# Kernel optimization log

Measured on AMD Instinct MI355X. Metric: run time of the kernel, lower is better.

The kernel has to match this reference:

```python
import jax, jax.numpy as jnp
import numpy as np

B, S, D, H = 8, 128, 256, 8
T = S + 1
HD = D // H  # head_dim = 32
GAMMA = 1.0
NEG_INF = -1e9
LN_EPS = 1e-5


def setup_inputs() -> dict:
    key = jax.random.key(0)
    ks = jax.random.split(key, 16)
    sc = 0.05
    return {
        "desc_embeddings": jax.random.normal(ks[0], (B, S, D), jnp.float32),
        "name_value_embeddings": jax.random.normal(ks[1], (B, T, D), jnp.float32),
        "prior_Q": jax.random.uniform(ks[2], (B, H, S, S), jnp.float32),
        "Wq": jax.random.normal(ks[3], (D, D), jnp.float32) * sc,
        "bq": jnp.zeros((D,), jnp.float32),
        "Wk": jax.random.normal(ks[4], (D, D), jnp.float32) * sc,
        "bk": jnp.zeros((D,), jnp.float32),
        "Wv": jax.random.normal(ks[5], (D, D), jnp.float32) * sc,
        "bv": jnp.zeros((D,), jnp.float32),
        "wa": jax.random.normal(ks[6], (3 * HD,), jnp.float32) * sc,  # attn_proj weight (out=1)
        "ba": jnp.zeros((), jnp.float32),
        "We1": jax.random.normal(ks[7], (2 * D, D), jnp.float32) * sc,
        "be1": jnp.zeros((D,), jnp.float32),
        "ln_g": jnp.ones((D,), jnp.float32),
        "ln_b": jnp.zeros((D,), jnp.float32),
        "We2": jax.random.normal(ks[8], (D, D), jnp.float32) * sc,
        "be2": jnp.zeros((D,), jnp.float32),
    }


def _layer_norm(x, g, b):
    mu = jnp.mean(x, axis=-1, keepdims=True)
    var = jnp.mean(jnp.square(x - mu), axis=-1, keepdims=True)
    return (x - mu) * jax.lax.rsqrt(var + LN_EPS) * g + b


def _heads(x, W, b):  # [B,T,D] -> [B,H,T,HD]
    return (x @ W + b).reshape(B, T, H, HD).transpose(0, 2, 1, 3)


def reference(desc_embeddings, name_value_embeddings, prior_Q,
              Wq, bq, Wk, bk, Wv, bv, wa, ba,
              We1, be1, ln_g, ln_b, We2, be2):
    # structural adjacency (same for every batch element): CLS->Var on, Var->CLS off,
    # Var-Var fully connected without self-loops
    adj = jnp.zeros((T, T), jnp.float32)
    adj = adj.at[1:, 1:].set(1.0 - jnp.eye(S, dtype=jnp.float32))
    adj = adj.at[0, 1:].set(1.0)

    q = _heads(name_value_embeddings, Wq, bq)  # [B,H,T,HD]
    k = _heads(name_value_embeddings, Wk, bk)
    v = _heads(name_value_embeddings, Wv, bv)

    # edge attributes: pairwise concat of desc embeddings, CLS rows/cols use [desc,desc]
    desc = desc_embeddings
    var_edge = jnp.concatenate([
        jnp.broadcast_to(desc[:, :, None, :], (B, S, S, D)),
        jnp.broadcast_to(desc[:, None, :, :], (B, S, S, D)),
    ], axis=-1)  # [B,S,S,2D]
    cls_edge = jnp.concatenate([desc, desc], axis=-1)  # [B,S,2D]
    edge = jnp.zeros((B, T, T, 2 * D), jnp.float32)
    edge = edge.at[:, 1:, 1:].set(var_edge)
    edge = edge.at[:, 0, 1:].set(cls_edge)
    edge = edge.at[:, 1:, 0].set(cls_edge)

    # edge_update MLP: Linear(2D->D) -> LayerNorm -> ReLU -> Linear(D->D)
    h = jax.nn.relu(_layer_norm(edge @ We1 + be1, ln_g, ln_b)) @ We2 + be2  # [B,T,T,D]
    # split into heads, mask by adjacency: [B,H,T,T,HD]
    edge_h = h.reshape(B, T, T, H, HD).transpose(0, 3, 1, 2, 4)
    edge_h = edge_h * adj[None, None, :, :, None]

    # gat_v1 + attn_proj(cat[q_i, k_j, e_ij]) is linear -> decompose to avoid
    # materializing the [B,H,T,T,3*HD] concat
    wa_q, wa_k, wa_e = wa[:HD], wa[HD:2 * HD], wa[2 * HD:]
    logits = (jnp.einsum('bhid,d->bhi', q, wa_q)[:, :, :, None]
              + jnp.einsum('bhjd,d->bhj', k, wa_k)[:, :, None, :]
              + jnp.einsum('bhijd,d->bhij', edge_h, wa_e)
              + ba)  # [B,H,T,T]

    # prior_Q logit-bias injection on Var-Var block
    eps = 1e-6
    p = jnp.clip(prior_Q, eps, 1.0 - eps)
    bias = (jnp.log(p) - jnp.log(1.0 - p)) * GAMMA  # [B,H,S,S]
    logits = logits.at[:, :, 1:, 1:].add(bias)

    # structural mask as pre-softmax -inf
    logits = logits + (adj == 0).astype(logits.dtype)[None, None] * NEG_INF

    attn = jax.nn.softmax(logits, axis=-1)  # [B,H,T,T]
    ctx = jnp.einsum('bhij,bhjd->bhid', attn, v)  # [B,H,T,HD]
    basis_outputs = ctx.transpose(0, 2, 1, 3)  # [B,T,H,HD]
    return basis_outputs, attn
```

## Files before the change

kernel.cpp:

```cpp
#include <hip/hip_runtime.h>
#include <math.h>

#define B 8
#define S 128
#define D 256
#define H 8
#define T 129
#define HD 32
#define BT (B*T)
#define NEG_INF -1000000000.0f
#define LN_EPS 1e-5f

__global__ __launch_bounds__(256) void prep_w(
    const float* __restrict__ Wq, const float* __restrict__ bq,
    const float* __restrict__ Wk, const float* __restrict__ bk,
    const float* __restrict__ We2, const float* __restrict__ be2,
    const float* __restrict__ wa,
    float* __restrict__ Wqk, float* __restrict__ bqk,
    float* __restrict__ W2aT, float* __restrict__ econst)
{
    int id = blockIdx.x * 256 + threadIdx.x;
    if (id < 2048) {
        int c = id >> 3, h = id & 7;
        float s = 0.f;
        #pragma unroll
        for (int d = 0; d < HD; ++d) s = fmaf(Wq[c*D + h*HD + d], wa[d], s);
        Wqk[c*16 + h] = s;
    } else if (id < 4096) {
        int id2 = id - 2048; int c = id2 >> 3, h = id2 & 7;
        float s = 0.f;
        #pragma unroll
        for (int d = 0; d < HD; ++d) s = fmaf(Wk[c*D + h*HD + d], wa[HD + d], s);
        Wqk[c*16 + 8 + h] = s;
    } else if (id < 6144) {
        int id2 = id - 4096; int h = id2 / D, c = id2 % D;
        float s = 0.f;
        #pragma unroll
        for (int d = 0; d < HD; ++d) s = fmaf(We2[c*D + h*HD + d], wa[2*HD + d], s);
        W2aT[h*D + c] = s;
    } else if (id < 6152) {
        int h = id - 6144;
        float s = 0.f;
        #pragma unroll
        for (int d = 0; d < HD; ++d) s = fmaf(bq[h*HD + d], wa[d], s);
        bqk[h] = s;
    } else if (id < 6160) {
        int h = id - 6152;
        float s = 0.f;
        #pragma unroll
        for (int d = 0; d < HD; ++d) s = fmaf(bk[h*HD + d], wa[HD + d], s);
        bqk[8 + h] = s;
    } else if (id < 6168) {
        int h = id - 6160;
        float s = 0.f;
        #pragma unroll
        for (int d = 0; d < HD; ++d) s = fmaf(be2[h*HD + d], wa[2*HD + d], s);
        econst[h] = s;
    }
}

__global__ __launch_bounds__(256) void gemm3(
    const float* __restrict__ nv, const float* __restrict__ desc,
    const float* __restrict__ Wv, const float* __restrict__ bv,
    const float* __restrict__ We1, const float* __restrict__ be1,
    const float* __restrict__ Wqk, const float* __restrict__ bqk,
    float* __restrict__ v, float* __restrict__ U, float* __restrict__ V,
    float* __restrict__ sU, float* __restrict__ sV, float* __restrict__ qdkdT)
{
    const int which = blockIdx.y;
    const int tid = threadIdx.x;
    __shared__ float xs[16][D];
    __shared__ float psum[4][8];

    if (which == 3) {
        if (blockIdx.x >= 65) return;
        const int r0 = blockIdx.x * 16;
        const int r = tid >> 4, c = tid & 15;
        for (int t = tid; t < 16 * D; t += 256) {
            int rr = r0 + (t >> 8);
            xs[t >> 8][t & 255] = (rr < BT) ? nv[rr * D + (t & 255)] : 0.f;
        }
        __syncthreads();
        float acc = 0.f;
        for (int kk = 0; kk < D; kk += 4) {
            float4 x = *(const float4*)&xs[r][kk];
            acc = fmaf(x.x, Wqk[(kk+0)*16 + c], acc);
            acc = fmaf(x.y, Wqk[(kk+1)*16 + c], acc);
            acc = fmaf(x.z, Wqk[(kk+2)*16 + c], acc);
            acc = fmaf(x.w, Wqk[(kk+3)*16 + c], acc);
        }
        const int rr = r0 + r;
        if (rr < BT) qdkdT[c*BT + rr] = acc + bqk[c];
        return;
    }

    const float* X; const float* W; const float* bias; float* out; int rows;
    if (which == 0)      { X = nv;   W = Wv;        bias = bv;  out = v; rows = BT; }
    else if (which == 1) { X = desc; W = We1;       bias = be1; out = U; rows = B*S; }
    else                 { X = desc; W = We1 + D*D; bias = nullptr; out = V; rows = B*S; }

    const int r0 = blockIdx.x * 8;
    if (r0 >= rows) return;

    #pragma unroll
    for (int r = 0; r < 8; ++r) {
        int rr = r0 + r;
        xs[r][tid] = (rr < rows) ? X[rr * D + tid] : 0.f;
    }
    __syncthreads();

    float acc[8] = {0.f,0.f,0.f,0.f,0.f,0.f,0.f,0.f};
    for (int kk = 0; kk < D; kk += 4) {
        float w0 = W[(kk+0)*D + tid];
        float w1 = W[(kk+1)*D + tid];
        float w2 = W[(kk+2)*D + tid];
        float w3 = W[(kk+3)*D + tid];
        #pragma unroll
        for (int r = 0; r < 8; ++r) {
            float4 x = *(const float4*)&xs[r][kk];
            acc[r] = fmaf(x.x, w0, acc[r]);
            acc[r] = fmaf(x.y, w1, acc[r]);
            acc[r] = fmaf(x.z, w2, acc[r]);
            acc[r] = fmaf(x.w, w3, acc[r]);
        }
    }
    const float bb = bias ? bias[tid] : 0.f;
    #pragma unroll
    for (int r = 0; r < 8; ++r) {
        int rr = r0 + r;
        if (rr < rows) out[rr * D + tid] = acc[r] + bb;
    }

    if (which >= 1) {
        const int wv = tid >> 6, ln = tid & 63;
        #pragma unroll
        for (int r = 0; r < 8; ++r) {
            float sps = acc[r] + bb;
            #pragma unroll
            for (int m = 32; m >= 1; m >>= 1) sps += __shfl_xor(sps, m);
            if (ln == 0) psum[wv][r] = sps;
        }
        __syncthreads();
        if (tid < 8) {
            float* dst = (which == 1) ? sU : sV;
            dst[r0 + tid] = psum[0][tid] + psum[1][tid] + psum[2][tid] + psum[3][tid];
        }
    }
}

__global__ __launch_bounds__(512, 4) void edge_attn(
    const float* __restrict__ U, const float* __restrict__ V,
    const float* __restrict__ W2aT, const float* __restrict__ econst,
    const float* __restrict__ ln_g, const float* __restrict__ ln_b,
    const float* __restrict__ qdkdT, const float* __restrict__ prior,
    const float* __restrict__ v, const float* __restrict__ ba,
    const float* __restrict__ sU, const float* __restrict__ sV,
    float* __restrict__ out_basis, float* __restrict__ out_attn)
{
    const int bid = blockIdx.x;
    const int b = bid / T, i = bid % T;
    const int tid = threadIdx.x, lane = tid & 63, wid = tid >> 6;
    const int c0 = lane * 4;

    __shared__ float escl[H][132];
    __shared__ float pat[H][132];

    const int h = wid;
    const int bh = b*H + h;
    const int j1 = 1 + lane, j2 = 65 + lane;
    const float qdv = qdkdT[h*BT + b*T + i];
    const float ba0 = ba[0];
    const float* kT = qdkdT + (8 + h)*BT + b*T;
    const float k1 = kT[j1], k2 = kT[j2];
    float lg1 = 0.f, lg2 = 0.f;
    if (i >= 1) {
        float pr = prior[((size_t)bh*S + (i-1))*S + (j1-1)];
        pr = fminf(fmaxf(pr, 1e-6f), 1.f - 1e-6f);
        lg1 = __logf(pr) - __logf(1.f - pr);
        pr = prior[((size_t)bh*S + (i-1))*S + (j2-1)];
        pr = fminf(fmaxf(pr, 1e-6f), 1.f - 1e-6f);
        lg2 = __logf(pr) - __logf(1.f - pr);
    }

    const float4 g4 = *(const float4*)(ln_g + c0);
    const float4 b4 = *(const float4*)(ln_b + c0);
    float4 w[H];
    #pragma unroll
    for (int hh = 0; hh < H; ++hh) w[hh] = *(const float4*)(W2aT + hh*D + c0);

    const bool i0 = (i == 0);
    float4 u4i = make_float4(0.f, 0.f, 0.f, 0.f);
    float sUi_s = 0.f;
    if (!i0) {
        u4i = *(const float4*)(U + (size_t)(b*S + (i-1))*D + c0);
        sUi_s = sU[b*S + (i-1)];
    }

    const bool bb0 = lane & 1, bb1 = lane & 2, bb2 = lane & 4;
    const bool bb3 = lane & 8, bb4 = lane & 16;
    const int hmap = 4*(lane&1) + 2*((lane>>1)&1) + ((lane>>2)&1);
    const float ech = econst[hmap];

    const int j0 = 1 + wid * 16;
    const float* Vb  = V + (size_t)(b*S + (j0-1))*D + c0;
    const float* Ub  = U + (size_t)(b*S + (j0-1))*D + c0;
    const float* sVb = sV + b*S + (j0-1);
    const float* sUb = sU + b*S + (j0-1);

    #pragma unroll 2
    for (int grp = 0; grp < 4; ++grp) {
        const int jb = grp * 4;
        float4 y0 = *(const float4*)(Vb + (size_t)(jb+0)*D);
        float4 y1 = *(const float4*)(Vb + (size_t)(jb+1)*D);
        float4 y2 = *(const float4*)(Vb + (size_t)(jb+2)*D);
        float4 y3 = *(const float4*)(Vb + (size_t)(jb+3)*D);
        const float4 sv4 = *(const float4*)(sVb + jb);
        float su0 = sUi_s, su1 = sUi_s, su2 = sUi_s, su3 = sUi_s;
        float4 u0 = u4i, u1 = u4i, u2 = u4i, u3 = u4i;
        if (i0) {
            u0 = *(const float4*)(Ub + (size_t)(jb+0)*D);
            u1 = *(const float4*)(Ub + (size_t)(jb+1)*D);
            u2 = *(const float4*)(Ub + (size_t)(jb+2)*D);
            u3 = *(const float4*)(Ub + (size_t)(jb+3)*D);
            const float4 su4 = *(const float4*)(sUb + jb);
            su0 = su4.x; su1 = su4.y; su2 = su4.z; su3 = su4.w;
        }
        y0.x += u0.x; y0.y += u0.y; y0.z += u0.z; y0.w += u0.w;
        y1.x += u1.x; y1.y += u1.y; y1.z += u1.z; y1.w += u1.w;
        y2.x += u2.x; y2.y += u2.y; y2.z += u2.z; y2.w += u2.w;
        y3.x += u3.x; y3.y += u3.y; y3.z += u3.z; y3.w += u3.w;

        float s2p0 = fmaf(y0.x,y0.x, fmaf(y0.y,y0.y, fmaf(y0.z,y0.z, y0.w*y0.w)));
        float s2p1 = fmaf(y1.x,y1.x, fmaf(y1.y,y1.y, fmaf(y1.z,y1.z, y1.w*y1.w)));
        float s2p2 = fmaf(y2.x,y2.x, fmaf(y2.y,y2.y, fmaf(y2.z,y2.z, y2.w*y2.w)));
        float s2p3 = fmaf(y3.x,y3.x, fmaf(y3.y,y3.y, fmaf(y3.z,y3.z, y3.w*y3.w)));
        float a0 = bb0 ? s2p2 : s2p0, d0 = bb0 ? s2p0 : s2p2;
        float a1 = bb0 ? s2p3 : s2p1, d1 = bb0 ? s2p1 : s2p3;
        float r0 = a0 + __shfl_xor(d0, 1);
        float r1 = a1 + __shfl_xor(d1, 1);
        float a2 = bb1 ? r1 : r0, d2 = bb1 ? r0 : r1;
        float z = a2 + __shfl_xor(d2, 2);
        z += __shfl_xor(z, 4);
        z += __shfl_xor(z, 8);
        z += __shfl_xor(z, 16);
        z += __shfl_xor(z, 32);
        const float mu0 = (su0 + sv4.x) * (1.f/D);
        const float mu1 = (su1 + sv4.y) * (1.f/D);
        const float mu2 = (su2 + sv4.z) * (1.f/D);
        const float mu3 = (su3 + sv4.w) * (1.f/D);
        const float musel = bb0 ? (bb1 ? mu3 : mu2) : (bb1 ? mu1 : mu0);
        const float var = fmaf(-musel, musel, z * (1.f/D));
        const float rsv = rsqrtf(var + LN_EPS);
        const float rA = __shfl_xor(rsv, 1);
        const float rB = __shfl_xor(rsv, 2);
        const float rC = __shfl_xor(rA, 2);
        const float rs0 = bb0 ? (bb1 ? rC : rA) : (bb1 ? rB : rsv);
        const float rs1 = bb0 ? (bb1 ? rA : rC) : (bb1 ? rsv : rB);
        const float rs2 = bb0 ? (bb1 ? rB : rsv) : (bb1 ? rC : rA);
        const float rs3 = bb0 ? (bb1 ? rsv : rB) : (bb1 ? rA : rC);

        float x0, x1, x2, x3;
        #define DO_J(YK, RSK, MUK, XOUT)                                          \
        {                                                                         \
            const float rg0 = RSK * g4.x, rg1 = RSK * g4.y;                       \
            const float rg2 = RSK * g4.z, rg3 = RSK * g4.w;                       \
            const float of0 = fmaf(-MUK, rg0, b4.x), of1 = fmaf(-MUK, rg1, b4.y); \
            const float of2 = fmaf(-MUK, rg2, b4.z), of3 = fmaf(-MUK, rg3, b4.w); \
            const float t0 = fmaxf(fmaf(YK.x, rg0, of0), 0.f);                    \
            const float t1 = fmaxf(fmaf(YK.y, rg1, of1), 0.f);                    \
            const float t2 = fmaxf(fmaf(YK.z, rg2, of2), 0.f);                    \
            const float t3 = fmaxf(fmaf(YK.w, rg3, of3), 0.f);                    \
            float ph0 = fmaf(t0, w[0].x, fmaf(t1, w[0].y, fmaf(t2, w[0].z, t3 * w[0].w))); \
            float ph1 = fmaf(t0, w[1].x, fmaf(t1, w[1].y, fmaf(t2, w[1].z, t3 * w[1].w))); \
            float ph2 = fmaf(t0, w[2].x, fmaf(t1, w[2].y, fmaf(t2, w[2].z, t3 * w[2].w))); \
            float ph3 = fmaf(t0, w[3].x, fmaf(t1, w[3].y, fmaf(t2, w[3].z, t3 * w[3].w))); \
            float ph4 = fmaf(t0, w[4].x, fmaf(t1, w[4].y, fmaf(t2, w[4].z, t3 * w[4].w))); \
            float ph5 = fmaf(t0, w[5].x, fmaf(t1, w[5].y, fmaf(t2, w[5].z, t3 * w[5].w))); \
            float ph6 = fmaf(t0, w[6].x, fmaf(t1, w[6].y, fmaf(t2, w[6].z, t3 * w[6].w))); \
            float ph7 = fmaf(t0, w[7].x, fmaf(t1, w[7].y, fmaf(t2, w[7].z, t3 * w[7].w))); \
            float e0 = bb0 ? ph4 : ph0, f0 = bb0 ? ph0 : ph4;                     \
            float e1 = bb0 ? ph5 : ph1, f1 = bb0 ? ph1 : ph5;                     \
            float e2 = bb0 ? ph6 : ph2, f2 = bb0 ? ph2 : ph6;                     \
            float e3 = bb0 ? ph7 : ph3, f3 = bb0 ? ph3 : ph7;                     \
            float p0 = e0 + __shfl_xor(f0, 1);                                    \
            float p1 = e1 + __shfl_xor(f1, 1);                                    \
            float p2 = e2 + __shfl_xor(f2, 1);                                    \
            float p3 = e3 + __shfl_xor(f3, 1);                                    \
            float q0 = (bb1 ? p2 : p0) + __shfl_xor(bb1 ? p0 : p2, 2);            \
            float q1 = (bb1 ? p3 : p1) + __shfl_xor(bb1 ? p1 : p3, 2);            \
            XOUT = (bb2 ? q1 : q0) + __shfl_xor(bb2 ? q0 : q1, 4);                \
        }
        DO_J(y0, rs0, mu0, x0)
        DO_J(y1, rs1, mu1, x1)
        DO_J(y2, rs2, mu2, x2)
        DO_J(y3, rs3, mu3, x3)
        #undef DO_J

        float tA0 = bb3 ? x2 : x0, sA0 = bb3 ? x0 : x2;
        float tA1 = bb3 ? x3 : x1, sA1 = bb3 ? x1 : x3;
        float w0t = tA0 + __shfl_xor(sA0, 8);
        float w1t = tA1 + __shfl_xor(sA1, 8);
        float zz = (bb4 ? w1t : w0t) + __shfl_xor(bb4 ? w0t : w1t, 16);
        zz += __shfl_xor(zz, 32);
        if (lane < 32) {
            const int jm = 2*((lane>>3)&1) + ((lane>>4)&1);
            escl[hmap][j0 + jb + jm] = zz + ech;
        }
    }
    __syncthreads();

    const bool val1 = !(i >= 1 && j1 == i);
    const bool val2 = !(i >= 1 && j2 == i);

    const float base = qdv + ba0;
    const float e1 = val1 ? __expf(base + k1 + escl[h][j1] + lg1) : 0.f;
    const float e2 = val2 ? __expf(base + k2 + escl[h][j2] + lg2) : 0.f;
    float ssum = e1 + e2;
    #pragma unroll
    for (int mm = 32; mm >= 1; mm >>= 1) ssum += __shfl_xor(ssum, mm);
    const float inv = 1.f / ssum;
    const float a1 = e1 * inv, a2 = e2 * inv;

    float* arow = out_attn + (size_t)(bh*T + i)*T;
    arow[j1] = a1;
    arow[j2] = a2;
    if (lane == 0) arow[0] = 0.f;
    pat[h][j1] = a1;
    pat[h][j2] = a2;

    const int dg = lane & 7;
    const int jg = lane >> 3;
    const float* vbase = v + (size_t)(b*T)*D + h*HD + dg*4;
    float4 acc4 = make_float4(0.f, 0.f, 0.f, 0.f);
    #pragma unroll
    for (int k = 0; k < 16; ++k) {
        const int j = 1 + k*8 + jg;
        const float p = pat[h][j];
        const float4 vv = *(const float4*)(vbase + (size_t)j*D);
        acc4.x = fmaf(p, vv.x, acc4.x);
        acc4.y = fmaf(p, vv.y, acc4.y);
        acc4.z = fmaf(p, vv.z, acc4.z);
        acc4.w = fmaf(p, vv.w, acc4.w);
    }
    #pragma unroll
    for (int mm = 8; mm <= 32; mm <<= 1) {
        acc4.x += __shfl_xor(acc4.x, mm);
        acc4.y += __shfl_xor(acc4.y, mm);
        acc4.z += __shfl_xor(acc4.z, mm);
        acc4.w += __shfl_xor(acc4.w, mm);
    }
    if (jg == 0)
        *(float4*)(out_basis + ((size_t)(b*T + i)*H + h)*HD + dg*4) = acc4;
}

extern "C" void kernel_launch(void* const* d_in, const int* in_sizes, int n_in,
                              void* d_out, int out_size, void* d_ws, size_t ws_size,
                              hipStream_t stream) {
    const float* desc  = (const float*)d_in[0];
    const float* nv    = (const float*)d_in[1];
    const float* prior = (const float*)d_in[2];
    const float* Wq  = (const float*)d_in[3];
    const float* bq  = (const float*)d_in[4];
    const float* Wk  = (const float*)d_in[5];
    const float* bk  = (const float*)d_in[6];
    const float* Wv  = (const float*)d_in[7];
    const float* bv  = (const float*)d_in[8];
    const float* wa  = (const float*)d_in[9];
    const float* ba  = (const float*)d_in[10];
    const float* We1 = (const float*)d_in[11];
    const float* be1 = (const float*)d_in[12];
    const float* lng = (const float*)d_in[13];
    const float* lnb = (const float*)d_in[14];
    const float* We2 = (const float*)d_in[15];
    const float* be2 = (const float*)d_in[16];

    float* ws = (float*)d_ws;
    float* U     = ws; ws += B*S*D;
    float* V     = ws; ws += B*S*D;
    float* v     = ws; ws += B*T*D;
    float* Wqk   = ws; ws += D*16;
    float* bqk   = ws; ws += 16;
    float* W2aT  = ws; ws += H*D;
    float* ec    = ws; ws += H;
    float* qdkdT = ws; ws += 16*BT;
    float* sU    = ws; ws += B*S;
    float* sV    = ws; ws += B*S;

    float* out_basis = (float*)d_out;
    float* out_attn  = out_basis + B*T*H*HD;

    prep_w<<<dim3(25), 256, 0, stream>>>(Wq, bq, Wk, bk, We2, be2, wa,
                                         Wqk, bqk, W2aT, ec);
    gemm3<<<dim3(129, 4), 256, 0, stream>>>(nv, desc, Wv, bv, We1, be1,
                                            Wqk, bqk, v, U, V, sU, sV, qdkdT);
    edge_attn<<<dim3(B*T), 512, 0, stream>>>(U, V, W2aT, ec, lng, lnb,
                                             qdkdT, prior, v, ba, sU, sV,
                                             out_basis, out_attn);
}
```

Baseline: 146.5 us.

## Fold weight prep into gemm3 and replace shuffle reduction with shared partial sums

Removes the separate prep_w launch. The per-block q/k attention-weight folding is recomputed redundantly in each gemm3 qdk block into shared memory, and the We2·wa folding runs as an extra blockIdx.y slice. In edge_attn, the final cross-lane shuffle tree for edge scores is replaced by writing per-octet partial sums to a larger shared buffer and summing 8 partials per j. This trades a kernel launch and some shuffles for redundant Wq/Wk reads per block and extra shared memory (about 34 KB) that may lower edge_attn occupancy.

After: 164.4 us. 1.12x slower.

```diff
diff --git a/kernel.cpp b/kernel.cpp
--- a/kernel.cpp
+++ b/kernel.cpp
@@ -11,66 +11,46 @@
 #define NEG_INF -1000000000.0f
 #define LN_EPS 1e-5f
 
-__global__ __launch_bounds__(256) void prep_w(
+__global__ __launch_bounds__(256) void gemm3(
+    const float* __restrict__ nv, const float* __restrict__ desc,
+    const float* __restrict__ Wv, const float* __restrict__ bv,
+    const float* __restrict__ We1, const float* __restrict__ be1,
     const float* __restrict__ Wq, const float* __restrict__ bq,
     const float* __restrict__ Wk, const float* __restrict__ bk,
     const float* __restrict__ We2, const float* __restrict__ be2,
     const float* __restrict__ wa,
-    float* __restrict__ Wqk, float* __restrict__ bqk,
-    float* __restrict__ W2aT, float* __restrict__ econst)
-{
-    int id = blockIdx.x * 256 + threadIdx.x;
-    if (id < 2048) {
-        int c = id >> 3, h = id & 7;
-        float s = 0.f;
-        #pragma unroll
-        for (int d = 0; d < HD; ++d) s = fmaf(Wq[c*D + h*HD + d], wa[d], s);
-        Wqk[c*16 + h] = s;
-    } else if (id < 4096) {
-        int id2 = id - 2048; int c = id2 >> 3, h = id2 & 7;
-        float s = 0.f;
-        #pragma unroll
-        for (int d = 0; d < HD; ++d) s = fmaf(Wk[c*D + h*HD + d], wa[HD + d], s);
-        Wqk[c*16 + 8 + h] = s;
-    } else if (id < 6144) {
-        int id2 = id - 4096; int h = id2 / D, c = id2 % D;
-        float s = 0.f;
-        #pragma unroll
-        for (int d = 0; d < HD; ++d) s = fmaf(We2[c*D + h*HD + d], wa[2*HD + d], s);
-        W2aT[h*D + c] = s;
-    } else if (id < 6152) {
-        int h = id - 6144;
-        float s = 0.f;
-        #pragma unroll
-        for (int d = 0; d < HD; ++d) s = fmaf(bq[h*HD + d], wa[d], s);
-        bqk[h] = s;
-    } else if (id < 6160) {
-        int h = id - 6152;
-        float s = 0.f;
-        #pragma unroll
-        for (int d = 0; d < HD; ++d) s = fmaf(bk[h*HD + d], wa[HD + d], s);
-        bqk[8 + h] = s;
-    } else if (id < 6168) {
-        int h = id - 6160;
-        float s = 0.f;
-        #pragma unroll
-        for (int d = 0; d < HD; ++d) s = fmaf(be2[h*HD + d], wa[2*HD + d], s);
-        econst[h] = s;
-    }
-}
-
-__global__ __launch_bounds__(256) void gemm3(
-    const float* __restrict__ nv, const float* __restrict__ desc,
-    const float* __restrict__ Wv, const float* __restrict__ bv,
-    const float* __restrict__ We1, const float* __restrict__ be1,
-    const float* __restrict__ Wqk, const float* __restrict__ bqk,
     float* __restrict__ v, float* __restrict__ U, float* __restrict__ V,
-    float* __restrict__ sU, float* __restrict__ sV, float* __restrict__ qdkdT)
+    float* __restrict__ sU, float* __restrict__ sV,
+    float* __restrict__ qdkdT, float* __restrict__ W2aT,
+    float* __restrict__ econst)
 {
     const int which = blockIdx.y;
     const int tid = threadIdx.x;
     __shared__ float xs[16][D];
     __shared__ float psum[4][8];
+    __shared__ float wqk_l[D][16];
+    __shared__ float bqk_l[16];
+
+    if (which == 4) {
+        if (blockIdx.x >= 9) return;
+        const int id = blockIdx.x * 256 + tid;
+        if (id < 2048) {
+            const int hh = id >> 8, c = id & 255;
+            float s = 0.f;
+            #pragma unroll
+            for (int d = 0; d < HD; ++d)
+                s = fmaf(We2[c*D + hh*HD + d], wa[2*HD + d], s);
+            W2aT[hh*D + c] = s;
+        } else if (id < 2056) {
+            const int hh = id - 2048;
+            float s = 0.f;
+            #pragma unroll
+            for (int d = 0; d < HD; ++d)
+                s = fmaf(be2[hh*HD + d], wa[2*HD + d], s);
+            econst[hh] = s;
+        }
+        return;
+    }
 
     if (which == 3) {
         if (blockIdx.x >= 65) return;
@@ -80,17 +60,43 @@
             int rr = r0 + (t >> 8);
             xs[t >> 8][t & 255] = (rr < BT) ? nv[rr * D + (t & 255)] : 0.f;
         }
+        #pragma unroll
+        for (int rep = 0; rep < 16; ++rep) {
+            const int idx = rep * 256 + tid;
+            const int cc = idx >> 4, hh = idx & 15;
+            const float* src  = (hh < 8) ? (Wq + cc*D + hh*HD)
+                                         : (Wk + cc*D + (hh-8)*HD);
+            const float* wsrc = (hh < 8) ? wa : (wa + HD);
+            float s = 0.f;
+            #pragma unroll
+            for (int d = 0; d < HD; d += 4) {
+                float4 a  = *(const float4*)(src + d);
+                float4 ww = *(const float4*)(wsrc + d);
+                s = fmaf(a.x, ww.x, fmaf(a.y, ww.y, fmaf(a.z, ww.z, fmaf(a.w, ww.w, s))));
+            }
+            wqk_l[cc][hh] = s;
+        }
+        if (tid < 16) {
+            const int hh = tid;
+            const float* src  = (hh < 8) ? (bq + hh*HD) : (bk + (hh-8)*HD);
+            const float* wsrc = (hh < 8) ? wa : (wa + HD);
+            float s = 0.f;
+            #pragma unroll
+            for (int d = 0; d < HD; ++d) s = fmaf(src[d], wsrc[d], s);
+            bqk_l[hh] = s;
+        }
         __syncthreads();
+
         float acc = 0.f;
         for (int kk = 0; kk < D; kk += 4) {
             float4 x = *(const float4*)&xs[r][kk];
-            acc = fmaf(x.x, Wqk[(kk+0)*16 + c], acc);
-            acc = fmaf(x.y, Wqk[(kk+1)*16 + c], acc);
-            acc = fmaf(x.z, Wqk[(kk+2)*16 + c], acc);
-            acc = fmaf(x.w, Wqk[(kk+3)*16 + c], acc);
+            acc = fmaf(x.x, wqk_l[kk+0][c], acc);
+            acc = fmaf(x.y, wqk_l[kk+1][c], acc);
+            acc = fmaf(x.z, wqk_l[kk+2][c], acc);
+            acc = fmaf(x.w, wqk_l[kk+3][c], acc);
         }
         const int rr = r0 + r;
-        if (rr < BT) qdkdT[c*BT + rr] = acc + bqk[c];
+        if (rr < BT) qdkdT[c*BT + rr] = acc + bqk_l[c];
         return;
     }
 
@@ -162,7 +168,7 @@
     const int tid = threadIdx.x, lane = tid & 63, wid = tid >> 6;
     const int c0 = lane * 4;
 
-    __shared__ float escl[H][132];
+    __shared__ float part[8 * 8 * 133];
     __shared__ float pat[H][132];
 
     const int h = wid;
@@ -170,6 +176,7 @@
     const int j1 = 1 + lane, j2 = 65 + lane;
     const float qdv = qdkdT[h*BT + b*T + i];
     const float ba0 = ba[0];
+    const float ech = econst[h];
     const float* kT = qdkdT + (8 + h)*BT + b*T;
     const float k1 = kT[j1], k2 = kT[j2];
     float lg1 = 0.f, lg2 = 0.f;
@@ -197,9 +204,8 @@
     }
 
     const bool bb0 = lane & 1, bb1 = lane & 2, bb2 = lane & 4;
-    const bool bb3 = lane & 8, bb4 = lane & 16;
     const int hmap = 4*(lane&1) + 2*((lane>>1)&1) + ((lane>>2)&1);
-    const float ech = econst[hmap];
+    const int pbase = (lane >> 3) * 1064 + hmap * 133;
 
     const int j0 = 1 + wid * 16;
     const float* Vb  = V + (size_t)(b*S + (j0-1))*D + c0;
@@ -296,25 +302,26 @@
         DO_J(y3, rs3, mu3, x3)
         #undef DO_J
 
-        float tA0 = bb3 ? x2 : x0, sA0 = bb3 ? x0 : x2;
-        float tA1 = bb3 ? x3 : x1, sA1 = bb3 ? x1 : x3;
-        float w0t = tA0 + __shfl_xor(sA0, 8);
-        float w1t = tA1 + __shfl_xor(sA1, 8);
-        float zz = (bb4 ? w1t : w0t) + __shfl_xor(bb4 ? w0t : w1t, 16);
-        zz += __shfl_xor(zz, 32);
-        if (lane < 32) {
-            const int jm = 2*((lane>>3)&1) + ((lane>>4)&1);
-            escl[hmap][j0 + jb + jm] = zz + ech;
-        }
+        part[pbase + j0 + jb + 0] = x0;
+        part[pbase + j0 + jb + 1] = x1;
+        part[pbase + j0 + jb + 2] = x2;
+        part[pbase + j0 + jb + 3] = x3;
     }
     __syncthreads();
 
     const bool val1 = !(i >= 1 && j1 == i);
     const bool val2 = !(i >= 1 && j2 == i);
 
-    const float base = qdv + ba0;
-    const float e1 = val1 ? __expf(base + k1 + escl[h][j1] + lg1) : 0.f;
-    const float e2 = val2 ? __expf(base + k2 + escl[h][j2] + lg2) : 0.f;
+    float sc1 = 0.f, sc2 = 0.f;
+    #pragma unroll
+    for (int oct = 0; oct < 8; ++oct) {
+        sc1 += part[oct*1064 + h*133 + j1];
+        sc2 += part[oct*1064 + h*133 + j2];
+    }
+
+    const float base = qdv + ba0 + ech;
+    const float e1 = val1 ? __expf(base + k1 + sc1 + lg1) : 0.f;
+    const float e2 = val2 ? __expf(base + k2 + sc2 + lg2) : 0.f;
     float ssum = e1 + e2;
     #pragma unroll
     for (int mm = 32; mm >= 1; mm >>= 1) ssum += __shfl_xor(ssum, mm);
@@ -378,8 +385,6 @@
     float* U     = ws; ws += B*S*D;
     float* V     = ws; ws += B*S*D;
     float* v     = ws; ws += B*T*D;
-    float* Wqk   = ws; ws += D*16;
-    float* bqk   = ws; ws += 16;
     float* W2aT  = ws; ws += H*D;
     float* ec    = ws; ws += H;
     float* qdkdT = ws; ws += 16*BT;
@@ -389,10 +394,9 @@
     float* out_basis = (float*)d_out;
     float* out_attn  = out_basis + B*T*H*HD;
 
-    prep_w<<<dim3(25), 256, 0, stream>>>(Wq, bq, Wk, bk, We2, be2, wa,
-                                         Wqk, bqk, W2aT, ec);
-    gemm3<<<dim3(129, 4), 256, 0, stream>>>(nv, desc, Wv, bv, We1, be1,
-                                            Wqk, bqk, v, U, V, sU, sV, qdkdT);
+    gemm3<<<dim3(129, 5), 256, 0, stream>>>(nv, desc, Wv, bv, We1, be1,
+                                            Wq, bq, Wk, bk, We2, be2, wa,
+                                            v, U, V, sU, sV, qdkdT, W2aT, ec);
     edge_attn<<<dim3(B*T), 512, 0, stream>>>(U, V, W2aT, ec, lng, lnb,
                                              qdkdT, prior, v, ba, sU, sV,
                                              out_basis, out_attn);
```
